# Performance work log

Hardware: AMD Instinct MI355X
Metric: run time of the kernel (lower is better)

## Reference

```python
import jax, jax.numpy as jnp
import numpy as np

DIM = 2048
NUM_HEADS = 16
NUM_KV_HEADS = 4
HEAD_DIM = DIM // NUM_HEADS  # 128
ROPE_BASE = 10000.0
CLIP = 31.0
BLOCK = 128


def fake_quant(w):
    """Blockwise int-ish fake quantization, steady QAT state (ratio=1, clip=31, no noise)."""
    out_f, in_f = w.shape
    pad = (-in_f) % BLOCK
    wp = jnp.pad(w, ((0, 0), (0, pad)))
    wb = wp.reshape(-1, BLOCK)
    # scale computed under no_grad in torch -> stop_gradient
    bmax = jnp.max(jnp.abs(wb), axis=1)
    s = jnp.maximum(bmax / CLIP, 1e-12).astype(jnp.float16)
    s = jnp.maximum(s, jnp.finfo(jnp.float16).tiny).astype(jnp.float32)
    s = jax.lax.stop_gradient(s)[:, None]
    ws = wb / s
    q = ws - jax.lax.stop_gradient(ws) + jax.lax.stop_gradient(
        jnp.round(jnp.clip(ws, -(CLIP + 1.0), CLIP)))  # STE
    qw = (q * s).reshape(out_f, in_f + pad)
    return qw[:, :in_f] if pad > 0 else qw


def rms_norm(x):
    eps = jnp.finfo(x.dtype).eps
    return x * jax.lax.rsqrt(jnp.mean(x * x, axis=-1, keepdims=True) + eps)


def rope_tables(seqlen, dtype):
    inv_freq = 1.0 / (ROPE_BASE ** (jnp.arange(0, HEAD_DIM, 2, dtype=jnp.float32) / HEAD_DIM))
    freqs = jnp.outer(jnp.arange(seqlen, dtype=jnp.float32), inv_freq)  # [S, hd/2]
    return jnp.cos(freqs).astype(dtype), jnp.sin(freqs).astype(dtype)


def apply_rotary(x, cos, sin):
    # x: [B,H,S,hd]; cos/sin: [S,hd/2]
    half = x.shape[-1] // 2
    x1, x2 = x[..., :half], x[..., half:]
    return jnp.concatenate((x1 * cos + x2 * sin, -x1 * sin + x2 * cos), axis=-1)


def setup_inputs() -> dict:
    key = jax.random.key(0)
    ks = jax.random.split(key, 6)
    kv_dim = NUM_KV_HEADS * HEAD_DIM
    std = DIM ** -0.5
    return {
        "x": jax.random.normal(ks[0], (2, 2048, DIM), dtype=jnp.float32),
        "Wq": jax.random.normal(ks[1], (DIM, DIM), dtype=jnp.float32) * std,
        "Wk": jax.random.normal(ks[2], (kv_dim, DIM), dtype=jnp.float32) * std,
        "Wv": jax.random.normal(ks[3], (kv_dim, DIM), dtype=jnp.float32) * std,
        "Wproj": jax.random.normal(ks[4], (DIM, DIM), dtype=jnp.float32) * std,
        "q_gain": jnp.full((NUM_HEADS,), 1.0, dtype=jnp.float32),
    }


def reference(x, Wq, Wk, Wv, Wproj, q_gain):
    B, S, D = x.shape
    H, KV, hd = NUM_HEADS, NUM_KV_HEADS, HEAD_DIM
    q = (x @ fake_quant(Wq).T).reshape(B, S, H, hd).transpose(0, 2, 1, 3)   # [B,H,S,hd]
    k = (x @ fake_quant(Wk).T).reshape(B, S, KV, hd).transpose(0, 2, 1, 3)  # [B,KV,S,hd]
    v = (x @ fake_quant(Wv).T).reshape(B, S, KV, hd).transpose(0, 2, 1, 3)
    q = rms_norm(q)
    k = rms_norm(k)
    cos, sin = rope_tables(S, q.dtype)
    q = apply_rotary(q, cos, sin)
    k = apply_rotary(k, cos, sin)
    q = q * q_gain[None, :, None, None]
    # GQA: expand kv heads
    rep = H // KV
    k = jnp.repeat(k, rep, axis=1)  # [B,H,S,hd]
    v = jnp.repeat(v, rep, axis=1)
    scale = 1.0 / jnp.sqrt(jnp.asarray(hd, dtype=q.dtype))
    scores = jnp.einsum("bhqd,bhkd->bhqk", q, k) * scale
    causal = jnp.tril(jnp.ones((S, S), dtype=bool))
    scores = jnp.where(causal, scores, jnp.asarray(-jnp.inf, dtype=scores.dtype))
    attn = jax.nn.softmax(scores, axis=-1)
    y = jnp.einsum("bhqk,bhkd->bhqd", attn, v)  # [B,H,S,hd]
    y = y.transpose(0, 2, 1, 3).reshape(B, S, D)
    return y @ fake_quant(Wproj).T
```

## Files before the change

### kernel.cpp

```cpp
#include <hip/hip_runtime.h>
#include <hip/hip_bf16.h>
#include <hip/hip_fp16.h>

#define SEQ    2048
#define DMODEL 2048
#define NH     16
#define NKV    4
#define HD     128
#define NTOT   3072
#define MROWS  4096

typedef __attribute__((ext_vector_type(4))) float f32x4;
typedef __attribute__((ext_vector_type(8))) __bf16 bf16x8;
typedef __attribute__((ext_vector_type(8))) unsigned short u16x8;
typedef __attribute__((ext_vector_type(4))) unsigned short u16x4;

__device__ __forceinline__ void async_copy16(const void* g, void* l) {
  __builtin_amdgcn_global_load_lds(
      (const __attribute__((address_space(1))) void*)g,
      (__attribute__((address_space(3))) void*)l, 16, 0, 0);
}

__device__ __forceinline__ unsigned short fto16(float f) {
  __hip_bfloat16 h = __float2bfloat16(f);
  return *(unsigned short*)&h;
}

__device__ __forceinline__ float b2f(unsigned short u) {
  unsigned int t = (unsigned int)u << 16;
  float f;
  __builtin_memcpy(&f, &t, 4);
  return f;
}

#define QSCALE 0.12751791437524245f
#define NEG_L2RB_64 (-0.2076205059304601f)

#define NFQ   20480
#define NCONV 8192
#define NROPE 512
__global__ __launch_bounds__(256) void prep_kernel(const float* __restrict__ Wq,
                                                   const float* __restrict__ Wk,
                                                   const float* __restrict__ Wv,
                                                   const float* __restrict__ Wp,
                                                   const float* __restrict__ x,
                                                   unsigned short* __restrict__ Wcat,
                                                   unsigned short* __restrict__ Wpq,
                                                   unsigned short* __restrict__ xb,
                                                   float* __restrict__ CS,
                                                   float* __restrict__ SN) {
  const int bid = blockIdx.x;
  const int tid = threadIdx.x;
  if (bid < NFQ) {
    int g = bid * 4 + (tid >> 6);
    int lane = tid & 63;
    const float* W;
    unsigned short* out;
    int blk;
    if (g < 32768)      { W = Wq; out = Wcat;                          blk = g; }
    else if (g < 40960) { W = Wk; out = Wcat + (size_t)2048 * 2048;    blk = g - 32768; }
    else if (g < 49152) { W = Wv; out = Wcat + (size_t)2560 * 2048;    blk = g - 40960; }
    else                { W = Wp; out = Wpq;                           blk = g - 49152; }
    const float* p = W + (size_t)blk * 128 + lane * 2;
    float w0 = p[0], w1 = p[1];
    float m = fmaxf(fabsf(w0), fabsf(w1));
#pragma unroll
    for (int o = 32; o; o >>= 1) m = fmaxf(m, __shfl_xor(m, o));
    float s = fmaxf(m / 31.0f, 1e-12f);
    s = __half2float(__float2half(s));
    s = fmaxf(s, 6.103515625e-05f);
    float q0 = rintf(fminf(fmaxf(w0 / s, -32.0f), 31.0f)) * s;
    float q1 = rintf(fminf(fmaxf(w1 / s, -32.0f), 31.0f)) * s;
    unsigned short* o16 = out + (size_t)blk * 128 + lane * 2;
    o16[0] = fto16(q0);
    o16[1] = fto16(q1);
  } else if (bid < NFQ + NCONV) {
    int i = ((bid - NFQ) * 256 + tid) * 4;
    float4 v = *(const float4*)(x + i);
    ushort4 o;
    o.x = fto16(v.x); o.y = fto16(v.y); o.z = fto16(v.z); o.w = fto16(v.w);
    *(ushort4*)(xb + i) = o;
  } else {
    int idx = (bid - NFQ - NCONV) * 256 + tid;
    int t = idx >> 6, l = idx & 63;
    float invf = exp2f((float)l * NEG_L2RB_64);
    float fr = (float)t * invf;
    CS[idx] = cosf(fr);
    SN[idx] = sinf(fr);
  }
}

#define BM 128
#define BN 128
#define BK 64
template <typename OT, bool FUSED>
__global__ __launch_bounds__(256, 3) void gemm_bt(const unsigned short* __restrict__ A,
                                                  const unsigned short* __restrict__ Bm,
                                                  OT* __restrict__ C,
                                                  unsigned short* __restrict__ vtb,
                                                  unsigned short* __restrict__ qbuf,
                                                  unsigned short* __restrict__ kbuf,
                                                  const float* __restrict__ qgain,
                                                  const float* __restrict__ CS,
                                                  const float* __restrict__ SN,
                                                  int M, int N, int K) {
  __shared__ unsigned short SH[FUSED ? 16896 : 16384];
  unsigned short* As = SH;
  unsigned short* Bs = SH + 8192;
  const int tid = threadIdx.x;
  const int wave = tid >> 6, lane = tid & 63;
  const int quad = lane >> 4, l16 = lane & 15;

  int wg = blockIdx.y * gridDim.x + blockIdx.x;
  int nwg = gridDim.x * gridDim.y;
  int cpx = nwg >> 3;
  int swz = (wg & 7) * cpx + (wg >> 3);
  int bxs = swz % gridDim.x, bys = swz / gridDim.x;
  const int m0 = bxs * BM, n0 = bys * BN;
  const int wm = (wave >> 1) * 64, wn = (wave & 1) * 64;

  const unsigned short* Ag = A + (size_t)m0 * K;
  const unsigned short* Bg = Bm + (size_t)n0 * K;

  f32x4 acc[4][4];
#pragma unroll
  for (int i = 0; i < 4; i++)
#pragma unroll
    for (int j = 0; j < 4; j++) acc[i][j] = f32x4{0.f, 0.f, 0.f, 0.f};

  const int srow = tid >> 3;
  const int sg8 = (((lane & 7) ^ (lane >> 3))) * 8;
  const unsigned short* gA = Ag + (size_t)srow * K + sg8;
  const unsigned short* gB = Bg + (size_t)srow * K + sg8;
  unsigned short* lA = &As[wave * 512];
  unsigned short* lB = &Bs[wave * 512];

  for (int k0 = 0; k0 < K; k0 += BK) {
    __syncthreads();
#pragma unroll
    for (int c = 0; c < 4; ++c) async_copy16(gA + (size_t)c * 32 * K + k0, lA + c * 2048);
#pragma unroll
    for (int c = 0; c < 4; ++c) async_copy16(gB + (size_t)c * 32 * K + k0, lB + c * 2048);
    __syncthreads();
#pragma unroll
    for (int kk = 0; kk < 2; ++kk) {
      bf16x8 af[4], bf[4];
#pragma unroll
      for (int t = 0; t < 4; t++)
        af[t] = *(const bf16x8*)&As[(wm + t * 16 + l16) * BK + ((((kk << 2) + quad) ^ (l16 & 7)) << 3)];
#pragma unroll
      for (int t = 0; t < 4; t++)
        bf[t] = *(const bf16x8*)&Bs[(wn + t * 16 + l16) * BK + ((((kk << 2) + quad) ^ (l16 & 7)) << 3)];
#pragma unroll
      for (int i = 0; i < 4; i++)
#pragma unroll
        for (int j = 0; j < 4; j++)
          acc[i][j] = __builtin_amdgcn_mfma_f32_16x16x32_bf16(af[i], bf[j], acc[i][j], 0, 0, 0);
    }
  }

  if constexpr (FUSED) {
    if (n0 >= 2560) {
      const int kvh = (n0 - 2560) >> 7;
#pragma unroll
      for (int i = 0; i < 4; i++) {
        int row0 = m0 + wm + i * 16 + quad * 4;
        int bz = row0 >> 11, s0 = row0 & 2047;
#pragma unroll
        for (int j = 0; j < 4; j++) {
          int d = wn + j * 16 + l16;
          u16x4 o;
#pragma unroll
          for (int r = 0; r < 4; r++) o[r] = fto16(acc[i][j][r]);
          *(u16x4*)&vtb[(size_t)((bz * NKV + kvh) * HD + d) * SEQ + s0] = o;
        }
      }
      return;
    }
    __syncthreads();
#pragma unroll
    for (int i = 0; i < 4; i++) {
      int tok0 = wm + i * 16 + quad * 4;
#pragma unroll
      for (int j = 0; j < 4; j++) {
        int d = wn + j * 16 + l16;
        u16x4 w;
#pragma unroll
        for (int r = 0; r < 4; r++) w[r] = fto16(acc[i][j][r]);
        *(u16x4*)&SH[d * 132 + tok0] = w;
      }
    }
    __syncthreads();
    const bool isq = (n0 < 2048);
    const int hh = isq ? (n0 >> 7) : ((n0 - 2048) >> 7);
    const float g = isq ? qgain[hh] * QSCALE : 1.0f;
#pragma unroll 1
    for (int gr = 0; gr < 8; ++gr) {
      int tk = wave * 32 + gr * 4;
      u16x4 a = *(const u16x4*)&SH[lane * 132 + tk];
      u16x4 b = *(const u16x4*)&SH[(lane + 64) * 132 + tk];
      float x1[4], x2[4], ss[4];
#pragma unroll
      for (int r = 0; r < 4; r++) {
        x1[r] = b2f(a[r]); x2[r] = b2f(b[r]);
        ss[r] = x1[r] * x1[r] + x2[r] * x2[r];
      }
#pragma unroll
      for (int o = 32; o; o >>= 1)
#pragma unroll
        for (int r = 0; r < 4; r++) ss[r] += __shfl_xor(ss[r], o);
#pragma unroll
      for (int r = 0; r < 4; r++) {
        int gt = m0 + tk + r;
        int bz = gt >> 11, tokg = gt & 2047;
        float rn = rsqrtf(ss[r] * (1.0f / 128.0f) + 1.1920929e-07f);
        float cs = CS[tokg * 64 + lane], sn = SN[tokg * 64 + lane];
        float n1 = x1[r] * rn, n2 = x2[r] * rn;
        unsigned short* dst = isq
            ? qbuf + ((size_t)(bz * NH + hh) * SEQ + tokg) * HD
            : kbuf + ((size_t)(bz * NKV + hh) * SEQ + tokg) * HD;
        dst[lane]      = fto16((n1 * cs + n2 * sn) * g);
        dst[lane + 64] = fto16((-n1 * sn + n2 * cs) * g);
      }
    }
    return;
  }

#pragma unroll
  for (int i = 0; i < 4; i++) {
    int row_base = m0 + wm + i * 16 + quad * 4;
#pragma unroll
    for (int j = 0; j < 4; j++) {
      int col = n0 + wn + j * 16 + l16;
#pragma unroll
      for (int r = 0; r < 4; r++) {
        if constexpr (sizeof(OT) == 2)
          C[(size_t)(row_base + r) * N + col] = fto16(acc[i][j][r]);
        else
          C[(size_t)(row_base + r) * N + col] = acc[i][j][r];
      }
    }
  }
}

__global__ __launch_bounds__(512, 4) void attn_kernel(const unsigned short* __restrict__ qb,
                                                      const unsigned short* __restrict__ kb,
                                                      const unsigned short* __restrict__ vtb,
                                                      unsigned short* __restrict__ yb) {
  __shared__ unsigned short Ks[2][64 * 128];
  __shared__ unsigned short Vt[128 * 64];
  __shared__ unsigned short Ps[8][16 * 64];

  const int bx = blockIdx.x;
  const int h = blockIdx.y;
  const int bz = blockIdx.z;
  const int qt = bz ? bx : (15 - bx);
  const int tid = threadIdx.x;
  const int wave = tid >> 6, lane = tid & 63;
  const int quad = lane >> 4, l16 = lane & 15;
  const int q0 = qt * 128;
  const int base = q0 + wave * 16;
  const int kdiag = base >> 6;

  const unsigned short* qg = qb + (size_t)(bz * NH + h) * SEQ * HD;
  const unsigned short* kg = kb + (size_t)(bz * NKV + (h >> 2)) * SEQ * HD;
  const unsigned short* vg = vtb + (size_t)(bz * NKV + (h >> 2)) * HD * SEQ;
  unsigned short* psw = &Ps[wave][0];

  bf16x8 qf[4];
#pragma unroll
  for (int ds = 0; ds < 4; ++ds)
    qf[ds] = *(const bf16x8*)(qg + (size_t)(base + l16) * HD + ds * 32 + quad * 8);

  f32x4 oacc[8];
#pragma unroll
  for (int j = 0; j < 8; ++j) oacc[j] = f32x4{0.f, 0.f, 0.f, 0.f};
  float m_i = -__builtin_inff();
  float l_i = 0.f;

  const int krow0 = wave * 4 + (lane >> 4);
  const int ksrcg = (lane & 15) ^ (krow0 & 15);
  const unsigned short* kgK = kg + (size_t)krow0 * HD + ksrcg * 8;

  const int vdw = tid >> 3, vgr = tid & 7;

  const int nkt = 2 * qt + 2;

  async_copy16(kgK, &Ks[0][wave * 512]);
  async_copy16(kgK + (size_t)32 * HD, &Ks[0][4096 + wave * 512]);
  u16x8 pv[2];
#pragma unroll
  for (int i = 0; i < 2; ++i)
    pv[i] = *(const u16x8*)(vg + (size_t)(i * 64 + vdw) * SEQ + vgr * 8);

  for (int kt = 0; kt < nkt; ++kt) {
    __syncthreads();
#pragma unroll
    for (int i = 0; i < 2; ++i) {
      int d = i * 64 + vdw;
      *(u16x8*)&Vt[d * 64 + ((vgr ^ (d & 7)) << 3)] = pv[i];
    }
    if (kt + 1 < nkt) {
      const unsigned short* s = kgK + (size_t)(kt + 1) * 64 * HD;
      async_copy16(s, &Ks[(kt + 1) & 1][wave * 512]);
      async_copy16(s + (size_t)32 * HD, &Ks[(kt + 1) & 1][4096 + wave * 512]);
    }
    __asm__ volatile("s_waitcnt lgkmcnt(0)" ::: "memory");
    __builtin_amdgcn_sched_barrier(0);
    __asm__ volatile("s_barrier" ::: "memory");

    if (kt + 1 < nkt) {
#pragma unroll
      for (int i = 0; i < 2; ++i)
        pv[i] = *(const u16x8*)(vg + (size_t)(i * 64 + vdw) * SEQ + (kt + 1) * 64 + vgr * 8);
    }

    if (kt <= kdiag) {
      const unsigned short* Kc = Ks[kt & 1];
      f32x4 st[4];
#pragma unroll
      for (int mt = 0; mt < 4; ++mt) st[mt] = f32x4{0.f, 0.f, 0.f, 0.f};
      __builtin_amdgcn_s_setprio(1);
#pragma unroll
      for (int mt = 0; mt < 4; ++mt)
#pragma unroll
        for (int ds = 0; ds < 4; ++ds) {
          bf16x8 kf = *(const bf16x8*)&Kc[(mt * 16 + l16) * 128 + ((((ds << 2) + quad) ^ l16) << 3)];
          st[mt] = __builtin_amdgcn_mfma_f32_16x16x32_bf16(kf, qf[ds], st[mt], 0, 0, 0);
        }
      __builtin_amdgcn_s_setprio(0);

      const int qrow = base + l16;
      float p[4][4];
      float mx = -__builtin_inff();
      if (kt == kdiag) {
#pragma unroll
        for (int mt = 0; mt < 4; ++mt)
#pragma unroll
          for (int r = 0; r < 4; ++r) {
            int kp = kt * 64 + mt * 16 + quad * 4 + r;
            float v = (kp <= qrow) ? st[mt][r] : -__builtin_inff();
            p[mt][r] = v;
            mx = fmaxf(mx, v);
          }
      } else {
#pragma unroll
        for (int mt = 0; mt < 4; ++mt)
#pragma unroll
          for (int r = 0; r < 4; ++r) {
            p[mt][r] = st[mt][r];
            mx = fmaxf(mx, st[mt][r]);
          }
      }
      mx = fmaxf(mx, __shfl_xor(mx, 16));
      mx = fmaxf(mx, __shfl_xor(mx, 32));
      float mnew = (mx > m_i + 8.f) ? mx : m_i;
      float rs = 0.f;
#pragma unroll
      for (int mt = 0; mt < 4; ++mt)
#pragma unroll
        for (int r = 0; r < 4; ++r) {
          float e = exp2f(p[mt][r] - mnew);
          p[mt][r] = e;
          rs += e;
        }
      rs += __shfl_xor(rs, 16);
      rs += __shfl_xor(rs, 32);
      if (mnew != m_i) {
        float a = exp2f(m_i - mnew);
#pragma unroll
        for (int j = 0; j < 8; ++j) oacc[j] *= a;
        l_i = l_i * a + rs;
        m_i = mnew;
      } else {
        l_i += rs;
      }

#pragma unroll
      for (int mt = 0; mt < 4; ++mt) {
        u16x4 w;
#pragma unroll
        for (int r = 0; r < 4; ++r) w[r] = fto16(p[mt][r]);
        int g = mt * 2 + (quad >> 1);
        *(u16x4*)&psw[l16 * 64 + ((g ^ (l16 & 7)) << 3) + (quad & 1) * 4] = w;
      }

      __asm__ volatile("s_waitcnt lgkmcnt(0)" ::: "memory");

      __builtin_amdgcn_s_setprio(1);
#pragma unroll
      for (int c = 0; c < 2; ++c) {
        bf16x8 pf = *(const bf16x8*)&psw[l16 * 64 + ((((c << 2) + quad) ^ (l16 & 7)) << 3)];
#pragma unroll
        for (int mt = 0; mt < 8; ++mt) {
          bf16x8 vf = *(const bf16x8*)&Vt[(mt * 16 + l16) * 64 + ((((c << 2) + quad) ^ (l16 & 7)) << 3)];
          oacc[mt] = __builtin_amdgcn_mfma_f32_16x16x32_bf16(vf, pf, oacc[mt], 0, 0, 0);
        }
      }
      __builtin_amdgcn_s_setprio(0);
    }
  }

  {
    float il = 1.0f / l_i;
    int qrow = base + l16;
#pragma unroll
    for (int mt = 0; mt < 8; ++mt) {
      u16x4 o;
#pragma unroll
      for (int r = 0; r < 4; ++r) o[r] = fto16(oacc[mt][r] * il);
      *(u16x4*)&yb[(size_t)(bz * SEQ + qrow) * DMODEL + h * HD + mt * 16 + quad * 4] = o;
    }
  }
}

extern "C" void kernel_launch(void* const* d_in, const int* in_sizes, int n_in,
                              void* d_out, int out_size, void* d_ws, size_t ws_size,
                              hipStream_t stream) {
  (void)in_sizes; (void)n_in; (void)out_size; (void)ws_size;
  const float* x  = (const float*)d_in[0];
  const float* Wq = (const float*)d_in[1];
  const float* Wk = (const float*)d_in[2];
  const float* Wv = (const float*)d_in[3];
  const float* Wp = (const float*)d_in[4];
  const float* qg = (const float*)d_in[5];
  float* out = (float*)d_out;
  char* ws = (char*)d_ws;

  unsigned short* xb   = (unsigned short*)(ws + 0);
  unsigned short* Wcat = (unsigned short*)(ws + 16777216);
  unsigned short* Wpq  = (unsigned short*)(ws + 29360128);
  float*          CS   = (float*)(ws + 37748736);
  float*          SN   = (float*)(ws + 38273024);
  unsigned short* qbuf = (unsigned short*)(ws + 62914560);
  unsigned short* kbuf = (unsigned short*)(ws + 79691776);
  unsigned short* vtb  = (unsigned short*)(ws + 83886080);
  unsigned short* yb   = xb;

  prep_kernel<<<NFQ + NCONV + NROPE, 256, 0, stream>>>(Wq, Wk, Wv, Wp, x,
                                                       Wcat, Wpq, xb, CS, SN);
  gemm_bt<unsigned short, true><<<dim3(32, 24), 256, 0, stream>>>(
      xb, Wcat, (unsigned short*)nullptr, vtb, qbuf, kbuf, qg, CS, SN,
      MROWS, NTOT, DMODEL);
  attn_kernel<<<dim3(16, NH, 2), 512, 0, stream>>>(qbuf, kbuf, vtb, yb);
  gemm_bt<float, false><<<dim3(32, 16), 256, 0, stream>>>(
      yb, Wpq, out, nullptr, nullptr, nullptr, nullptr, nullptr, nullptr,
      MROWS, DMODEL, DMODEL);
}
```

Baseline: 292.2 us.

## Split long causal query tiles across two KV chunks with a combine kernel

The last four query tiles of each head, which have the most causal key tiles, are each split into two blocks covering halves of the KV range. Each half writes unnormalized fp32 partial outputs plus running max and sum to workspace, and a new combine kernel merges them with log-sum-exp weights into the bf16 output. This is meant to shorten the critical-path blocks and even out load across the grid. The cost is an extra kernel launch and the fp32 partial traffic through global memory.

```diff
diff --git a/kernel.cpp b/kernel.cpp
--- a/kernel.cpp
+++ b/kernel.cpp
@@ -246,7 +246,9 @@
 __global__ __launch_bounds__(512, 4) void attn_kernel(const unsigned short* __restrict__ qb,
                                                       const unsigned short* __restrict__ kb,
                                                       const unsigned short* __restrict__ vtb,
-                                                      unsigned short* __restrict__ yb) {
+                                                      unsigned short* __restrict__ yb,
+                                                      float* __restrict__ Opart,
+                                                      float* __restrict__ mlb) {
   __shared__ unsigned short Ks[2][64 * 128];
   __shared__ unsigned short Vt[128 * 64];
   __shared__ unsigned short Ps[8][16 * 64];
@@ -254,12 +256,24 @@
   const int bx = blockIdx.x;
   const int h = blockIdx.y;
   const int bz = blockIdx.z;
-  const int qt = bz ? bx : (15 - bx);
   const int tid = threadIdx.x;
   const int wave = tid >> 6, lane = tid & 63;
   const int quad = lane >> 4, l16 = lane & 15;
-  const int q0 = qt * 128;
-  const int base = q0 + wave * 16;
+
+  int qt, k0, k1, cchunk = -1, qi = 0;
+  if (bx < 12) {
+    qt = bz ? bx : (11 - bx);
+    k0 = 0; k1 = 2 * qt + 2;
+  } else {
+    int idx = bx - 12;
+    qi = idx >> 1; cchunk = idx & 1;
+    qt = 12 + qi;
+    int nkt = 2 * qt + 2, half = nkt >> 1;
+    k0 = cchunk ? half : 0;
+    k1 = cchunk ? nkt : half;
+  }
+
+  const int base = qt * 128 + wave * 16;
   const int kdiag = base >> 6;
 
   const unsigned short* qg = qb + (size_t)(bz * NH + h) * SEQ * HD;
@@ -284,23 +298,21 @@
 
   const int vdw = tid >> 3, vgr = tid & 7;
 
-  const int nkt = 2 * qt + 2;
-
-  async_copy16(kgK, &Ks[0][wave * 512]);
-  async_copy16(kgK + (size_t)32 * HD, &Ks[0][4096 + wave * 512]);
+  async_copy16(kgK + (size_t)k0 * 64 * HD, &Ks[k0 & 1][wave * 512]);
+  async_copy16(kgK + (size_t)(k0 * 64 + 32) * HD, &Ks[k0 & 1][4096 + wave * 512]);
   u16x8 pv[2];
 #pragma unroll
   for (int i = 0; i < 2; ++i)
-    pv[i] = *(const u16x8*)(vg + (size_t)(i * 64 + vdw) * SEQ + vgr * 8);
-
-  for (int kt = 0; kt < nkt; ++kt) {
+    pv[i] = *(const u16x8*)(vg + (size_t)(i * 64 + vdw) * SEQ + k0 * 64 + vgr * 8);
+
+  for (int kt = k0; kt < k1; ++kt) {
     __syncthreads();
 #pragma unroll
     for (int i = 0; i < 2; ++i) {
       int d = i * 64 + vdw;
       *(u16x8*)&Vt[d * 64 + ((vgr ^ (d & 7)) << 3)] = pv[i];
     }
-    if (kt + 1 < nkt) {
+    if (kt + 1 < k1) {
       const unsigned short* s = kgK + (size_t)(kt + 1) * 64 * HD;
       async_copy16(s, &Ks[(kt + 1) & 1][wave * 512]);
       async_copy16(s + (size_t)32 * HD, &Ks[(kt + 1) & 1][4096 + wave * 512]);
@@ -309,7 +321,7 @@
     __builtin_amdgcn_sched_barrier(0);
     __asm__ volatile("s_barrier" ::: "memory");
 
-    if (kt + 1 < nkt) {
+    if (kt + 1 < k1) {
 #pragma unroll
       for (int i = 0; i < 2; ++i)
         pv[i] = *(const u16x8*)(vg + (size_t)(i * 64 + vdw) * SEQ + (kt + 1) * 64 + vgr * 8);
@@ -401,6 +413,20 @@
     }
   }
 
+  if (cchunk >= 0) {
+    const int rloc = wave * 16 + l16;
+    float* op = Opart + ((size_t)(((cchunk * 2 + bz) * NH + h) * 4 + qi) * 128 + rloc) * 128;
+#pragma unroll
+    for (int mt = 0; mt < 8; ++mt)
+      *(f32x4*)&op[mt * 16 + quad * 4] = oacc[mt];
+    if (quad == 0) {
+      float* ml = mlb + (size_t)(((cchunk * 2 + bz) * NH + h) * 4 + qi) * 256;
+      ml[rloc] = m_i;
+      ml[128 + rloc] = l_i;
+    }
+    return;
+  }
+
   {
     float il = 1.0f / l_i;
     int qrow = base + l16;
@@ -411,6 +437,39 @@
       for (int r = 0; r < 4; ++r) o[r] = fto16(oacc[mt][r] * il);
       *(u16x4*)&yb[(size_t)(bz * SEQ + qrow) * DMODEL + h * HD + mt * 16 + quad * 4] = o;
     }
+  }
+}
+
+__global__ __launch_bounds__(256) void combine_kernel(const float* __restrict__ Opart,
+                                                      const float* __restrict__ mlb,
+                                                      unsigned short* __restrict__ yb) {
+  const int qi = blockIdx.x & 3;
+  const int h = (blockIdx.x >> 2) & 15;
+  const int bz = blockIdx.x >> 6;
+  const int q = threadIdx.x >> 1;
+  const int dh = (threadIdx.x & 1) * 64;
+
+  const size_t i0 = (size_t)(((0 * 2 + bz) * NH + h) * 4 + qi);
+  const size_t i1 = (size_t)(((1 * 2 + bz) * NH + h) * 4 + qi);
+  const float m1 = mlb[i0 * 256 + q],     l1 = mlb[i0 * 256 + 128 + q];
+  const float m2 = mlb[i1 * 256 + q],     l2 = mlb[i1 * 256 + 128 + q];
+  const float mm = fmaxf(m1, m2);
+  float w1 = exp2f(m1 - mm), w2 = exp2f(m2 - mm);
+  const float il = 1.0f / (l1 * w1 + l2 * w2);
+  w1 *= il; w2 *= il;
+
+  const float* o1 = Opart + (i0 * 128 + q) * 128;
+  const float* o2 = Opart + (i1 * 128 + q) * 128;
+  const int qrow = (12 + qi) * 128 + q;
+  unsigned short* dst = yb + (size_t)(bz * SEQ + qrow) * DMODEL + h * HD;
+#pragma unroll
+  for (int d0 = 0; d0 < 64; d0 += 4) {
+    f32x4 a = *(const f32x4*)&o1[dh + d0];
+    f32x4 b = *(const f32x4*)&o2[dh + d0];
+    u16x4 o;
+#pragma unroll
+    for (int r = 0; r < 4; ++r) o[r] = fto16(a[r] * w1 + b[r] * w2);
+    *(u16x4*)&dst[dh + d0] = o;
   }
 }
 
@@ -432,6 +491,8 @@
   unsigned short* Wpq  = (unsigned short*)(ws + 29360128);
   float*          CS   = (float*)(ws + 37748736);
   float*          SN   = (float*)(ws + 38273024);
+  float*          Opart= (float*)(ws + 38797312);
+  float*          mlb  = (float*)(ws + 55574528);
   unsigned short* qbuf = (unsigned short*)(ws + 62914560);
   unsigned short* kbuf = (unsigned short*)(ws + 79691776);
   unsigned short* vtb  = (unsigned short*)(ws + 83886080);
@@ -442,7 +503,8 @@
   gemm_bt<unsigned short, true><<<dim3(32, 24), 256, 0, stream>>>(
       xb, Wcat, (unsigned short*)nullptr, vtb, qbuf, kbuf, qg, CS, SN,
       MROWS, NTOT, DMODEL);
-  attn_kernel<<<dim3(16, NH, 2), 512, 0, stream>>>(qbuf, kbuf, vtb, yb);
+  attn_kernel<<<dim3(20, NH, 2), 512, 0, stream>>>(qbuf, kbuf, vtb, yb, Opart, mlb);
+  combine_kernel<<<128, 256, 0, stream>>>(Opart, mlb, yb);
   gemm_bt<float, false><<<dim3(32, 16), 256, 0, stream>>>(
       yb, Wpq, out, nullptr, nullptr, nullptr, nullptr, nullptr, nullptr,
       MROWS, DMODEL, DMODEL);
```

Result: slower. 307.5 us (+5.2%).
